# Optimization experiments

Measured on AMD Instinct MI355X. Metric: run time of the kernel, lower is better.

Reference implementation:

```python
import jax, jax.numpy as jnp
import numpy as np

F = 256   # num_features
H = 64    # num_hidden_features
B = 8192  # batch


def setup_inputs() -> dict:
    key = jax.random.key(0)
    ks = jax.random.split(key, 7)
    s1 = 1.0  # torch Linear init scale ~ U(-1/sqrt(fan_in), ...); use normal*1/sqrt(fan_in)
    sH = 1.0 / np.sqrt(H)
    x = jax.random.normal(ks[0], (B, F), dtype=jnp.float32)
    # Stacked per-feature weights. torch Linear: y = x @ W.T + b, W:[out,in].
    w1 = jax.random.normal(ks[1], (F, H), dtype=jnp.float32) * s1      # [F, H]  (in=1)
    b1 = jax.random.normal(ks[2], (F, H), dtype=jnp.float32) * s1
    w2 = jax.random.normal(ks[3], (F, H, H), dtype=jnp.float32) * sH   # [F, out, in]
    b2 = jax.random.normal(ks[4], (F, H), dtype=jnp.float32) * sH
    w3 = jax.random.normal(ks[5], (F, H), dtype=jnp.float32) * sH      # [F, H] (out=1)
    b3 = jax.random.normal(ks[6], (F,), dtype=jnp.float32) * sH
    return {"x": x, "w1": w1, "b1": b1, "w2": w2, "b2": b2, "w3": w3, "b3": b3}


def reference(x, w1, b1, w2, b2, w3, b3):
    # x: [B, F]; per-feature MLP 1 -> H -> H -> 1, fused via batched einsums.
    h1 = jax.nn.relu(x[:, :, None] * w1[None, :, :] + b1[None])        # [B, F, H]
    h2 = jax.nn.relu(jnp.einsum('bfh,foh->bfo', h1, w2) + b2[None])    # [B, F, H]
    out = jnp.einsum('bfh,fh->bf', h2, w3) + b3[None]                  # [B, F]
    return out
```

## Files before the change

### kernel.cpp

```cpp
#include <hip/hip_runtime.h>
#include <hip/hip_bf16.h>


namespace {

constexpr int kF = 256;
constexpr int kH = 64;
constexpr int kB = 8192;

constexpr int kFPB     = 4;
constexpr int kRPB     = 512;
constexpr int kThreads = 256;
constexpr int kFG      = kF / kFPB;
constexpr int kRG      = kB / kRPB;
constexpr int kBlocks  = kFG * kRG;
constexpr int kPasses  = kRPB / 16;

using f32x4  = __attribute__((ext_vector_type(4))) float;
using bf16x4 = __attribute__((ext_vector_type(4))) __bf16;
using bf16x8 = __attribute__((ext_vector_type(8))) __bf16;

__global__ __launch_bounds__(kThreads, 4)
void mlp_pf_v4(const float* __restrict__ x,
               const float* __restrict__ w1,
               const float* __restrict__ b1,
               const float* __restrict__ w2,
               const float* __restrict__ b2,
               const float* __restrict__ w3,
               const float* __restrict__ b3,
               float* __restrict__ out)
{
  __shared__ float xs[kFPB][kRPB];
  __shared__ float outb[kRPB][kFPB + 1];

  const int tid  = (int)threadIdx.x;
  const int wid  = tid >> 6;
  const int lane = tid & 63;
  const int l15  = lane & 15;
  const int lg   = lane >> 4;

  const int fg = (int)blockIdx.x & (kFG - 1);
  const int rg = (int)blockIdx.x >> 6;
  const int f  = fg * kFPB + wid;
  const int r0 = rg * kRPB;

  bf16x8 w2frag[4][2];
  {
    const float* w2f = w2 + (size_t)f * (kH * kH);
    #pragma unroll
    for (int t = 0; t < 4; ++t) {
      const int o = t * 16 + l15;
      #pragma unroll
      for (int ks = 0; ks < 2; ++ks) {
        const float* p = w2f + o * kH + ks * 32 + lg * 8;
        const f32x4 lo = *reinterpret_cast<const f32x4*>(p);
        const f32x4 hi = *reinterpret_cast<const f32x4*>(p + 4);
        w2frag[t][ks] = __builtin_shufflevector(
            __builtin_convertvector(lo, bf16x4),
            __builtin_convertvector(hi, bf16x4), 0, 1, 2, 3, 4, 5, 6, 7);
      }
    }
  }

  #pragma unroll
  for (int rr = tid; rr < kRPB; rr += kThreads) {
    const f32x4 v = *reinterpret_cast<const f32x4*>(
        x + (size_t)(r0 + rr) * kF + fg * kFPB);
    xs[0][rr] = v[0]; xs[1][rr] = v[1]; xs[2][rr] = v[2]; xs[3][rr] = v[3];
  }

  f32x4 w1v[2][2], b1v[2][2];
  #pragma unroll
  for (int ks = 0; ks < 2; ++ks) {
    const float* pw = w1 + f * kH + ks * 32 + lg * 8;
    const float* pb = b1 + f * kH + ks * 32 + lg * 8;
    w1v[ks][0] = *reinterpret_cast<const f32x4*>(pw);
    w1v[ks][1] = *reinterpret_cast<const f32x4*>(pw + 4);
    b1v[ks][0] = *reinterpret_cast<const f32x4*>(pb);
    b1v[ks][1] = *reinterpret_cast<const f32x4*>(pb + 4);
  }
  f32x4 b2c[4], w3v[4];
  #pragma unroll
  for (int t = 0; t < 4; ++t) {
    b2c[t] = *reinterpret_cast<const f32x4*>(b2 + f * kH + t * 16 + lg * 4);
    w3v[t] = *reinterpret_cast<const f32x4*>(w3 + f * kH + t * 16 + lg * 4);
  }
  const float b3v = b3[f];

  __syncthreads();

  const f32x4 zero4 = {0.f, 0.f, 0.f, 0.f};

  #pragma unroll 4
  for (int p = 0; p < kPasses; ++p) {
    const float xv = xs[wid][p * 16 + l15];

    bf16x8 h1frag[2];
    #pragma unroll
    for (int ks = 0; ks < 2; ++ks) {
      f32x4 a = w1v[ks][0] * xv + b1v[ks][0];
      f32x4 b = w1v[ks][1] * xv + b1v[ks][1];
      a = __builtin_elementwise_max(a, zero4);
      b = __builtin_elementwise_max(b, zero4);
      h1frag[ks] = __builtin_shufflevector(
          __builtin_convertvector(a, bf16x4),
          __builtin_convertvector(b, bf16x4), 0, 1, 2, 3, 4, 5, 6, 7);
    }

    f32x4 p4 = zero4;
    #pragma unroll
    for (int t = 0; t < 4; ++t) {
      f32x4 acc = __builtin_amdgcn_mfma_f32_16x16x32_bf16(
          w2frag[t][0], h1frag[0], b2c[t], 0, 0, 0);
      acc = __builtin_amdgcn_mfma_f32_16x16x32_bf16(
          w2frag[t][1], h1frag[1], acc, 0, 0, 0);
      const f32x4 r = __builtin_elementwise_max(acc, zero4);
      p4 += r * w3v[t];
    }

    float s = (p4[0] + p4[1]) + (p4[2] + p4[3]);
    s += __shfl_xor(s, 16);
    s += __shfl_xor(s, 32);

    if (lg == 0) outb[p * 16 + l15][wid] = s + b3v;
  }

  __syncthreads();

  #pragma unroll
  for (int rr = tid; rr < kRPB; rr += kThreads) {
    const f32x4 v = {outb[rr][0], outb[rr][1], outb[rr][2], outb[rr][3]};
    *reinterpret_cast<f32x4*>(out + (size_t)(r0 + rr) * kF + fg * kFPB) = v;
  }
}

}

extern "C" void kernel_launch(void* const* d_in, const int* in_sizes, int n_in,
                              void* d_out, int out_size, void* d_ws, size_t ws_size,
                              hipStream_t stream) {
  const float* x  = (const float*)d_in[0];
  const float* w1 = (const float*)d_in[1];
  const float* b1 = (const float*)d_in[2];
  const float* w2 = (const float*)d_in[3];
  const float* b2 = (const float*)d_in[4];
  const float* w3 = (const float*)d_in[5];
  const float* b3 = (const float*)d_in[6];
  float* out = (float*)d_out;

  hipLaunchKernelGGL(mlp_pf_v4, dim3(kBlocks), dim3(kThreads), 0, stream,
                     x, w1, b1, w2, b2, w3, b3, out);
}
```

Baseline: 43.44 us.

## Halve rows per block, vectorize x reads, defer cross-lane reduction to epilogue

```diff
diff --git a/kernel.cpp b/kernel.cpp
--- a/kernel.cpp
+++ b/kernel.cpp
@@ -9,19 +9,23 @@
 constexpr int kB = 8192;
 
 constexpr int kFPB     = 4;
-constexpr int kRPB     = 512;
+constexpr int kRPB     = 256;
 constexpr int kThreads = 256;
 constexpr int kFG      = kF / kFPB;
 constexpr int kRG      = kB / kRPB;
 constexpr int kBlocks  = kFG * kRG;
 constexpr int kPasses  = kRPB / 16;
+constexpr int kQ       = kPasses / 4;
+
+constexpr int kXPad = 20;
+constexpr int kOPad = kRPB + 1;
 
 using f32x4  = __attribute__((ext_vector_type(4))) float;
 using bf16x4 = __attribute__((ext_vector_type(4))) __bf16;
 using bf16x8 = __attribute__((ext_vector_type(8))) __bf16;
 
 __global__ __launch_bounds__(kThreads, 4)
-void mlp_pf_v4(const float* __restrict__ x,
+void mlp_pf_v5(const float* __restrict__ x,
                const float* __restrict__ w1,
                const float* __restrict__ b1,
                const float* __restrict__ w2,
@@ -30,8 +34,8 @@
                const float* __restrict__ b3,
                float* __restrict__ out)
 {
-  __shared__ float xs[kFPB][kRPB];
-  __shared__ float outb[kRPB][kFPB + 1];
+  __shared__ float xs[kFPB][16][kXPad];
+  __shared__ float ob[kFPB * 4][kOPad];
 
   const int tid  = (int)threadIdx.x;
   const int wid  = tid >> 6;
@@ -62,11 +66,13 @@
     }
   }
 
-  #pragma unroll
-  for (int rr = tid; rr < kRPB; rr += kThreads) {
+  {
+    const int rr = tid;
     const f32x4 v = *reinterpret_cast<const f32x4*>(
         x + (size_t)(r0 + rr) * kF + fg * kFPB);
-    xs[0][rr] = v[0]; xs[1][rr] = v[1]; xs[2][rr] = v[2]; xs[3][rr] = v[3];
+    const int a = rr & 15, b = rr >> 4;
+    xs[0][a][b] = v[0]; xs[1][a][b] = v[1];
+    xs[2][a][b] = v[2]; xs[3][a][b] = v[3];
   }
 
   f32x4 w1v[2][2], b1v[2][2];
@@ -85,51 +91,60 @@
     b2c[t] = *reinterpret_cast<const f32x4*>(b2 + f * kH + t * 16 + lg * 4);
     w3v[t] = *reinterpret_cast<const f32x4*>(w3 + f * kH + t * 16 + lg * 4);
   }
-  const float b3v = b3[f];
 
   __syncthreads();
 
   const f32x4 zero4 = {0.f, 0.f, 0.f, 0.f};
+  float* obp = &ob[wid * 4 + lg][l15];
 
-  #pragma unroll 4
-  for (int p = 0; p < kPasses; ++p) {
-    const float xv = xs[wid][p * 16 + l15];
+  #pragma unroll
+  for (int q = 0; q < kQ; ++q) {
+    const f32x4 xq = *reinterpret_cast<const f32x4*>(&xs[wid][l15][q * 4]);
 
-    bf16x8 h1frag[2];
     #pragma unroll
-    for (int ks = 0; ks < 2; ++ks) {
-      f32x4 a = w1v[ks][0] * xv + b1v[ks][0];
-      f32x4 b = w1v[ks][1] * xv + b1v[ks][1];
-      a = __builtin_elementwise_max(a, zero4);
-      b = __builtin_elementwise_max(b, zero4);
-      h1frag[ks] = __builtin_shufflevector(
-          __builtin_convertvector(a, bf16x4),
-          __builtin_convertvector(b, bf16x4), 0, 1, 2, 3, 4, 5, 6, 7);
+    for (int j = 0; j < 4; ++j) {
+      const int p = q * 4 + j;
+      const float xv = xq[j];
+
+      bf16x8 h1frag[2];
+      #pragma unroll
+      for (int ks = 0; ks < 2; ++ks) {
+        f32x4 a = w1v[ks][0] * xv + b1v[ks][0];
+        f32x4 b = w1v[ks][1] * xv + b1v[ks][1];
+        a = __builtin_elementwise_max(a, zero4);
+        b = __builtin_elementwise_max(b, zero4);
+        h1frag[ks] = __builtin_shufflevector(
+            __builtin_convertvector(a, bf16x4),
+            __builtin_convertvector(b, bf16x4), 0, 1, 2, 3, 4, 5, 6, 7);
+      }
+
+      f32x4 p4 = zero4;
+      #pragma unroll
+      for (int t = 0; t < 4; ++t) {
+        f32x4 acc = __builtin_amdgcn_mfma_f32_16x16x32_bf16(
+            w2frag[t][0], h1frag[0], b2c[t], 0, 0, 0);
+        acc = __builtin_amdgcn_mfma_f32_16x16x32_bf16(
+            w2frag[t][1], h1frag[1], acc, 0, 0, 0);
+        const f32x4 r = __builtin_elementwise_max(acc, zero4);
+        p4 += r * w3v[t];
+      }
+
+      obp[p * 16] = (p4[0] + p4[1]) + (p4[2] + p4[3]);
     }
-
-    f32x4 p4 = zero4;
-    #pragma unroll
-    for (int t = 0; t < 4; ++t) {
-      f32x4 acc = __builtin_amdgcn_mfma_f32_16x16x32_bf16(
-          w2frag[t][0], h1frag[0], b2c[t], 0, 0, 0);
-      acc = __builtin_amdgcn_mfma_f32_16x16x32_bf16(
-          w2frag[t][1], h1frag[1], acc, 0, 0, 0);
-      const f32x4 r = __builtin_elementwise_max(acc, zero4);
-      p4 += r * w3v[t];
-    }
-
-    float s = (p4[0] + p4[1]) + (p4[2] + p4[3]);
-    s += __shfl_xor(s, 16);
-    s += __shfl_xor(s, 32);
-
-    if (lg == 0) outb[p * 16 + l15][wid] = s + b3v;
   }
 
   __syncthreads();
 
-  #pragma unroll
-  for (int rr = tid; rr < kRPB; rr += kThreads) {
-    const f32x4 v = {outb[rr][0], outb[rr][1], outb[rr][2], outb[rr][3]};
+  {
+    const int rr = tid;
+    const f32x4 b3q = *reinterpret_cast<const f32x4*>(b3 + fg * kFPB);
+    f32x4 v;
+    #pragma unroll
+    for (int w = 0; w < 4; ++w) {
+      const float s0 = ob[w * 4 + 0][rr] + ob[w * 4 + 1][rr];
+      const float s1 = ob[w * 4 + 2][rr] + ob[w * 4 + 3][rr];
+      v[w] = s0 + s1 + b3q[w];
+    }
     *reinterpret_cast<f32x4*>(out + (size_t)(r0 + rr) * kF + fg * kFPB) = v;
   }
 }
@@ -148,6 +163,6 @@
   const float* b3 = (const float*)d_in[6];
   float* out = (float*)d_out;
 
-  hipLaunchKernelGGL(mlp_pf_v4, dim3(kBlocks), dim3(kThreads), 0, stream,
+  hipLaunchKernelGGL(mlp_pf_v5, dim3(kBlocks), dim3(kThreads), 0, stream,
                      x, w1, b1, w2, b2, w3, b3, out);
 }
```

Result: slower. 101.7 us (+134.1%).
